# Performance work log

Hardware: AMD Instinct MI355X
Metric: run time of the kernel (lower is better)

The kernel has to match this reference:

```python
import jax, jax.numpy as jnp
import numpy as np

EPS = 1e-5
NEG_SLOPE = 0.01

def leaky_relu(x):
    return jnp.where(x > 0, x, NEG_SLOPE * x)

def graph_conv(x, src, dst, ew, W, n_nodes):
    # DGL GraphConv, norm='both', bias=False, with edge_weight.
    ones = jnp.ones(src.shape[0], dtype=x.dtype)
    out_deg = jax.ops.segment_sum(ones, src, num_segments=n_nodes)
    in_deg = jax.ops.segment_sum(ones, dst, num_segments=n_nodes)
    out_n = jnp.where(out_deg > 0, out_deg, 1.0) ** -0.5
    in_n = jnp.where(in_deg > 0, in_deg, 1.0) ** -0.5
    xs = x * out_n[:, None]
    msg = xs[src] * ew[:, None]              # [E, F] gather + elementwise
    agg = jax.ops.segment_sum(msg, dst, num_segments=n_nodes)  # scatter-add
    return (agg * in_n[:, None]) @ W

def graph_norm(x, gamma, beta, alpha):
    # GraphNorm called without graph arg -> normalize over all nodes per feature
    mean = jnp.mean(x, axis=0, keepdims=True)
    sub = x - alpha * mean
    var = jnp.mean(sub * sub, axis=0, keepdims=True)
    return gamma * sub * jax.lax.rsqrt(var + EPS) + beta

def inst_norm(x):
    # InstanceNorm1d(affine=False) on 2D [B,C]: normalize each row over features
    m = jnp.mean(x, axis=1, keepdims=True)
    v = jnp.mean((x - m) ** 2, axis=1, keepdims=True)
    return (x - m) * jax.lax.rsqrt(v + EPS)

def segment_mean(x, seg, num_segments):
    s = jax.ops.segment_sum(x, seg, num_segments=num_segments)
    c = jax.ops.segment_sum(jnp.ones(x.shape[0], x.dtype), seg, num_segments=num_segments)
    return s / jnp.maximum(c, 1.0)[:, None]

def setup_inputs() -> dict:
    N, E, B = 50000, 800000, 50
    IN, H, OUT = 64, 128, 16
    key = jax.random.key(0)
    ks = jax.random.split(key, 16)
    inp = {
        "node_feats": jax.random.normal(ks[0], (N, IN), jnp.float32),
        "src": jax.random.randint(ks[1], (E,), 0, N, jnp.int32),
        "dst": jax.random.randint(ks[2], (E,), 0, N, jnp.int32),
        "edge_weight": jax.random.uniform(ks[3], (E,), jnp.float32),
        "graph_id": jnp.sort(jax.random.randint(ks[4], (N,), 0, B, jnp.int32)),
        "W1": jax.random.normal(ks[5], (IN, H), jnp.float32) * (2.0 / IN) ** 0.5,
        "gn1_gamma": jnp.ones((H,), jnp.float32),
        "gn1_beta": jnp.zeros((H,), jnp.float32),
        "gn1_alpha": jnp.ones((H,), jnp.float32),
        "W2": jax.random.normal(ks[6], (H, H // 2), jnp.float32) * (2.0 / H) ** 0.5,
        "gn2_gamma": jnp.ones((H // 2,), jnp.float32),
        "gn2_beta": jnp.zeros((H // 2,), jnp.float32),
        "gn2_alpha": jnp.ones((H // 2,), jnp.float32),
        "L1": jax.random.normal(ks[7], (H // 2, H // 4), jnp.float32) * (1.0 / (H // 2)) ** 0.5,
        "L2": jax.random.normal(ks[8], (H // 4, H // 8), jnp.float32) * (1.0 / (H // 4)) ** 0.5,
        "L3": jax.random.normal(ks[9], (H // 8, H // 16), jnp.float32) * (1.0 / (H // 8)) ** 0.5,
        "Wc": jax.random.normal(ks[10], (H // 16, OUT), jnp.float32) * (1.0 / (H // 16)) ** 0.5,
    }
    return inp

def reference(node_feats, src, dst, edge_weight, graph_id,
              W1, gn1_gamma, gn1_beta, gn1_alpha,
              W2, gn2_gamma, gn2_beta, gn2_alpha,
              L1, L2, L3, Wc):
    N = node_feats.shape[0]
    B = 50
    h = graph_conv(node_feats, src, dst, edge_weight, W1, N)
    h = graph_norm(leaky_relu(h), gn1_gamma, gn1_beta, gn1_alpha)
    h = graph_conv(h, src, dst, edge_weight, W2, N)
    h = graph_norm(leaky_relu(h), gn2_gamma, gn2_beta, gn2_alpha)
    g = segment_mean(h, graph_id, B)          # mean_nodes readout -> [B, H/2]
    g = inst_norm(leaky_relu(g @ L1))          # dropout is identity in eval
    g = inst_norm(leaky_relu(g @ L2))
    g = inst_norm(leaky_relu(g @ L3))
    return g @ Wc
```

## Files before the change

### kernel.cpp

```cpp
#include <hip/hip_runtime.h>
#include <hip/hip_bf16.h>

#define NEG_SLOPE 0.01f
#define EPS 1e-5f

__device__ __forceinline__ float leaky(float x){ return x > 0.f ? x : NEG_SLOPE * x; }

__global__ void deg_kernel(const int* __restrict__ src, const int* __restrict__ dst,
                           int* __restrict__ iout, int* __restrict__ iin, int E){
  int e = blockIdx.x * blockDim.x + threadIdx.x;
  if (e < E){
    atomicAdd(&iout[src[e]], 1);
    atomicAdd(&iin[dst[e]], 1);
  }
}

__global__ void norm_kernel(const int* __restrict__ iout, const int* __restrict__ iin,
                            float* __restrict__ out_n, float* __restrict__ in_n, int N){
  int i = blockIdx.x * blockDim.x + threadIdx.x;
  if (i < N){
    int a = iout[i], b = iin[i];
    out_n[i] = rsqrtf((float)(a > 0 ? a : 1));
    in_n[i]  = rsqrtf((float)(b > 0 ? b : 1));
  }
}

__global__ __launch_bounds__(256) void scan_blocksum(const int* __restrict__ iin,
                                                     int* __restrict__ bsum, int N){
  __shared__ int sm[256];
  int t = threadIdx.x;
  int i = blockIdx.x * 256 + t;
  sm[t] = (i < N) ? iin[i] : 0;
  __syncthreads();
  for (int off = 128; off > 0; off >>= 1){
    if (t < off) sm[t] += sm[t + off];
    __syncthreads();
  }
  if (t == 0) bsum[blockIdx.x] = sm[0];
}

__global__ __launch_bounds__(1024) void scan_offsets(const int* __restrict__ bsum,
    int* __restrict__ boff, int nb, int* __restrict__ row_ptr, int N){
  __shared__ int sm[1024];
  int t = threadIdx.x;
  sm[t] = (t < nb) ? bsum[t] : 0;
  __syncthreads();
  for (int off = 1; off < 1024; off <<= 1){
    int v = (t >= off) ? sm[t - off] : 0;
    __syncthreads();
    sm[t] += v;
    __syncthreads();
  }
  if (t < nb) boff[t] = (t == 0) ? 0 : sm[t - 1];
  if (t == 1023) row_ptr[N] = sm[1023];
}

__global__ __launch_bounds__(256) void scan_write(const int* __restrict__ iin,
    const int* __restrict__ boff, int* __restrict__ row_ptr, int* __restrict__ cursor, int N){
  __shared__ int sm[256];
  int t = threadIdx.x;
  int i = blockIdx.x * 256 + t;
  int v = (i < N) ? iin[i] : 0;
  sm[t] = v;
  __syncthreads();
  for (int off = 1; off < 256; off <<= 1){
    int u = (t >= off) ? sm[t - off] : 0;
    __syncthreads();
    sm[t] += u;
    __syncthreads();
  }
  int excl = sm[t] - v + boff[blockIdx.x];
  if (i < N){ row_ptr[i] = excl; cursor[i] = excl; }
}

__global__ void fill_kernel(const int* __restrict__ src, const int* __restrict__ dst,
                            const float* __restrict__ ew, int* __restrict__ cursor,
                            int* __restrict__ esrc, float* __restrict__ eww, int E){
  int e = blockIdx.x * blockDim.x + threadIdx.x;
  if (e < E){
    int d = dst[e];
    int pos = atomicAdd(&cursor[d], 1);
    esrc[pos] = src[e];
    eww[pos] = ew[e];
  }
}

template<int MODE>
__global__ __launch_bounds__(256) void agg_csr(const float* __restrict__ xin,
    const int* __restrict__ row_ptr, const int* __restrict__ esrc,
    const float* __restrict__ eww, const float* __restrict__ out_n,
    const float* __restrict__ in_n, float* __restrict__ outp, int N){
  int node = (int)((blockIdx.x * (unsigned)blockDim.x + threadIdx.x) >> 6);
  int f = threadIdx.x & 63;
  if (node >= N) return;
  int e0 = row_ptr[node], e1 = row_ptr[node + 1];
  float acc = 0.f;
  #pragma unroll 2
  for (int e = e0; e < e1; ++e){
    int s = esrc[e];
    float w = eww[e];
    if (MODE == 1) w *= out_n[s];
    acc += xin[(size_t)s * 64 + f] * w;
  }
  acc *= in_n[node];
  if (MODE == 2) acc = leaky(acc);
  outp[(size_t)node * 64 + f] = acc;
}

__global__ __launch_bounds__(256) void gemm1_kernel(const float* __restrict__ agg,
    const float* __restrict__ W1, float* __restrict__ h1, int N){
  __shared__ float sW[64 * 128];
  __shared__ float sIn[64][64];
  int t = threadIdx.x;
  for (int i = t; i < 64 * 128 / 4; i += 256)
    ((float4*)sW)[i] = ((const float4*)W1)[i];
  int r0 = blockIdx.x * 64;
  for (int i = t; i < 64 * 16; i += 256){
    int r = i >> 4, q = i & 15;
    int row = r0 + r;
    float4 v = make_float4(0.f, 0.f, 0.f, 0.f);
    if (row < N) v = ((const float4*)(agg + (size_t)row * 64))[q];
    ((float4*)&sIn[r][0])[q] = v;
  }
  __syncthreads();
  int cp = t & 63;
  int rg = t >> 6;
  float2 acc[16];
  #pragma unroll
  for (int j = 0; j < 16; ++j) acc[j] = make_float2(0.f, 0.f);
  const float2* sW2 = (const float2*)sW;
  for (int k = 0; k < 64; k += 4){
    float2 w0 = sW2[(k + 0) * 64 + cp];
    float2 w1 = sW2[(k + 1) * 64 + cp];
    float2 w2 = sW2[(k + 2) * 64 + cp];
    float2 w3 = sW2[(k + 3) * 64 + cp];
    #pragma unroll
    for (int j = 0; j < 16; ++j){
      float4 a = *(const float4*)&sIn[rg * 16 + j][k];
      acc[j].x += a.x * w0.x + a.y * w1.x + a.z * w2.x + a.w * w3.x;
      acc[j].y += a.x * w0.y + a.y * w1.y + a.z * w2.y + a.w * w3.y;
    }
  }
  #pragma unroll
  for (int j = 0; j < 16; ++j){
    int row = r0 + rg * 16 + j;
    if (row < N){
      float2 o = make_float2(leaky(acc[j].x), leaky(acc[j].y));
      ((float2*)(h1 + (size_t)row * 128))[cp] = o;
    }
  }
}

template<int F>
__global__ void colstats_kernel(const float* __restrict__ h, int N,
                                float* __restrict__ sum, float* __restrict__ sumsq){
  int f = threadIdx.x;
  float s = 0.f, s2 = 0.f;
  for (int r = blockIdx.x; r < N; r += gridDim.x){
    float v = h[(size_t)r * F + f];
    s += v; s2 += v * v;
  }
  atomicAdd(&sum[f], s);
  atomicAdd(&sumsq[f], s2);
}

__global__ void finalize_norm(const float* __restrict__ sum, const float* __restrict__ sumsq,
                              const float* __restrict__ gamma, const float* __restrict__ beta,
                              const float* __restrict__ alpha,
                              float* __restrict__ a, float* __restrict__ b, int F, float invN){
  int f = threadIdx.x;
  if (f < F){
    float m = sum[f] * invN;
    float ex2 = sumsq[f] * invN;
    float al = alpha[f];
    float var = ex2 - m * m * al * (2.f - al);
    float av = gamma[f] * rsqrtf(var + EPS);
    a[f] = av;
    b[f] = beta[f] - av * al * m;
  }
}

__global__ __launch_bounds__(256) void gemm2_kernel(const float* __restrict__ h1,
    const float* __restrict__ out_n, const float* __restrict__ a1, const float* __restrict__ b1,
    const float* __restrict__ W2, float* __restrict__ z, int N){
  __shared__ float sW[128 * 64];
  __shared__ float sIn[64][128];
  int t = threadIdx.x;
  for (int i = t; i < 128 * 64 / 4; i += 256)
    ((float4*)sW)[i] = ((const float4*)W2)[i];
  int r0 = blockIdx.x * 64;
  for (int i = t; i < 64 * 32; i += 256){
    int r = i >> 5, q = i & 31;
    int row = r0 + r;
    float4 v = make_float4(0.f, 0.f, 0.f, 0.f);
    if (row < N){
      float4 h  = ((const float4*)(h1 + (size_t)row * 128))[q];
      float4 av = ((const float4*)a1)[q];
      float4 bv = ((const float4*)b1)[q];
      float  on = out_n[row];
      v.x = (av.x * h.x + bv.x) * on;
      v.y = (av.y * h.y + bv.y) * on;
      v.z = (av.z * h.z + bv.z) * on;
      v.w = (av.w * h.w + bv.w) * on;
    }
    ((float4*)&sIn[r][0])[q] = v;
  }
  __syncthreads();
  int cp = t & 31;
  int rg = t >> 5;
  float2 acc[8];
  #pragma unroll
  for (int j = 0; j < 8; ++j) acc[j] = make_float2(0.f, 0.f);
  const float2* sW2 = (const float2*)sW;
  for (int k = 0; k < 128; k += 4){
    float2 w0 = sW2[(k + 0) * 32 + cp];
    float2 w1 = sW2[(k + 1) * 32 + cp];
    float2 w2 = sW2[(k + 2) * 32 + cp];
    float2 w3 = sW2[(k + 3) * 32 + cp];
    #pragma unroll
    for (int j = 0; j < 8; ++j){
      float4 a = *(const float4*)&sIn[rg * 8 + j][k];
      acc[j].x += a.x * w0.x + a.y * w1.x + a.z * w2.x + a.w * w3.x;
      acc[j].y += a.x * w0.y + a.y * w1.y + a.z * w2.y + a.w * w3.y;
    }
  }
  #pragma unroll
  for (int j = 0; j < 8; ++j){
    int row = r0 + rg * 8 + j;
    if (row < N) ((float2*)(z + (size_t)row * 64))[cp] = acc[j];
  }
}

__global__ void post2_kernel(const float* __restrict__ hv, const int* __restrict__ gid,
                             int N, int chunk,
                             float* __restrict__ sum2, float* __restrict__ sumsq2,
                             float* __restrict__ segsum, float* __restrict__ cnt){
  int f = threadIdx.x;
  int r0 = blockIdx.x * chunk;
  int r1 = min(N, r0 + chunk);
  if (r0 >= r1) return;
  float s = 0.f, s2 = 0.f;
  int cur = gid[r0];
  float seg = 0.f;
  int run = 0;
  for (int r = r0; r < r1; ++r){
    int g = gid[r];
    if (g != cur){
      atomicAdd(&segsum[(size_t)cur * 64 + f], seg);
      if (f == 0) atomicAdd(&cnt[cur], (float)run);
      seg = 0.f; run = 0; cur = g;
    }
    float v = hv[(size_t)r * 64 + f];
    s += v; s2 += v * v;
    seg += v; ++run;
  }
  atomicAdd(&segsum[(size_t)cur * 64 + f], seg);
  if (f == 0) atomicAdd(&cnt[cur], (float)run);
  atomicAdd(&sum2[f], s);
  atomicAdd(&sumsq2[f], s2);
}

__global__ void head_kernel(const float* __restrict__ segsum, const float* __restrict__ cnt,
                            const float* __restrict__ a2, const float* __restrict__ b2,
                            const float* __restrict__ L1, const float* __restrict__ L2,
                            const float* __restrict__ L3, const float* __restrict__ Wc,
                            float* __restrict__ out){
  __shared__ float bufA[64];
  __shared__ float bufB[32];
  __shared__ float bufC[8];
  int b = blockIdx.x;
  int j = threadIdx.x;
  float c = cnt[b];
  float g0 = (c > 0.f) ? (a2[j] * (segsum[(size_t)b * 64 + j] / c) + b2[j]) : 0.f;
  bufA[j] = g0;
  __syncthreads();
  float y = 0.f;
  if (j < 32){
    float acc = 0.f;
    for (int f = 0; f < 64; ++f) acc += bufA[f] * L1[f * 32 + j];
    y = leaky(acc);
  }
  float m = y;
  for (int mask = 1; mask <= 16; mask <<= 1) m += __shfl_xor(m, mask);
  m *= (1.f / 32.f);
  float d = y - m;
  float v = d * d;
  for (int mask = 1; mask <= 16; mask <<= 1) v += __shfl_xor(v, mask);
  v *= (1.f / 32.f);
  float yn = d * rsqrtf(v + EPS);
  if (j < 32) bufB[j] = yn;
  __syncthreads();
  y = 0.f;
  if (j < 16){
    float acc = 0.f;
    for (int f = 0; f < 32; ++f) acc += bufB[f] * L2[f * 16 + j];
    y = leaky(acc);
  }
  m = y;
  for (int mask = 1; mask <= 8; mask <<= 1) m += __shfl_xor(m, mask);
  m *= (1.f / 16.f);
  d = y - m; v = d * d;
  for (int mask = 1; mask <= 8; mask <<= 1) v += __shfl_xor(v, mask);
  v *= (1.f / 16.f);
  yn = d * rsqrtf(v + EPS);
  if (j < 16) bufA[j] = yn;
  __syncthreads();
  y = 0.f;
  if (j < 8){
    float acc = 0.f;
    for (int f = 0; f < 16; ++f) acc += bufA[f] * L3[f * 8 + j];
    y = leaky(acc);
  }
  m = y;
  for (int mask = 1; mask <= 4; mask <<= 1) m += __shfl_xor(m, mask);
  m *= (1.f / 8.f);
  d = y - m; v = d * d;
  for (int mask = 1; mask <= 4; mask <<= 1) v += __shfl_xor(v, mask);
  v *= (1.f / 8.f);
  yn = d * rsqrtf(v + EPS);
  if (j < 8) bufC[j] = yn;
  __syncthreads();
  if (j < 16){
    float acc = 0.f;
    for (int f = 0; f < 8; ++f) acc += bufC[f] * Wc[f * 16 + j];
    out[(size_t)b * 16 + j] = acc;
  }
}

extern "C" void kernel_launch(void* const* d_in, const int* in_sizes, int n_in,
                              void* d_out, int out_size, void* d_ws, size_t ws_size,
                              hipStream_t stream){
  const float* x   = (const float*)d_in[0];
  const int*   src = (const int*)  d_in[1];
  const int*   dst = (const int*)  d_in[2];
  const float* ew  = (const float*)d_in[3];
  const int*   gid = (const int*)  d_in[4];
  const float* W1  = (const float*)d_in[5];
  const float* g1  = (const float*)d_in[6];
  const float* be1 = (const float*)d_in[7];
  const float* al1 = (const float*)d_in[8];
  const float* W2  = (const float*)d_in[9];
  const float* g2  = (const float*)d_in[10];
  const float* be2 = (const float*)d_in[11];
  const float* al2 = (const float*)d_in[12];
  const float* L1  = (const float*)d_in[13];
  const float* L2  = (const float*)d_in[14];
  const float* L3  = (const float*)d_in[15];
  const float* Wc  = (const float*)d_in[16];
  int N = in_sizes[0] / 64;
  int E = in_sizes[1];
  const int B = 50;
  int nb = (N + 255) / 256;

  char* wsb = (char*)d_ws;
  size_t off = 0;
  int* iout    = (int*)(wsb + off); off += sizeof(int) * (size_t)N;
  int* iin     = (int*)(wsb + off); off += sizeof(int) * (size_t)N;
  int* row_ptr = (int*)(wsb + off); off += sizeof(int) * ((size_t)N + 1);
  int* bsum    = (int*)(wsb + off); off += sizeof(int) * 1024;
  int* boff    = (int*)(wsb + off); off += sizeof(int) * 1024;
  int* esrc    = (int*)(wsb + off); off += sizeof(int) * (size_t)E;
  float* eww   = (float*)(wsb + off); off += sizeof(float) * (size_t)E;
  float* out_n = (float*)(wsb + off); off += sizeof(float) * (size_t)N;
  float* in_n  = (float*)(wsb + off); off += sizeof(float) * (size_t)N;
  float* P     = (float*)(wsb + off); off += sizeof(float) * (size_t)N * 64;
  float* H     = (float*)(wsb + off); off += sizeof(float) * (size_t)N * 128;
  float* sum1  = (float*)(wsb + off); off += sizeof(float) * 128;
  float* sumsq1= (float*)(wsb + off); off += sizeof(float) * 128;
  float* a1    = (float*)(wsb + off); off += sizeof(float) * 128;
  float* b1    = (float*)(wsb + off); off += sizeof(float) * 128;
  float* sum2  = (float*)(wsb + off); off += sizeof(float) * 64;
  float* sumsq2= (float*)(wsb + off); off += sizeof(float) * 64;
  float* a2    = (float*)(wsb + off); off += sizeof(float) * 64;
  float* b2    = (float*)(wsb + off); off += sizeof(float) * 64;
  float* segsum= (float*)(wsb + off); off += sizeof(float) * (size_t)B * 64;
  float* cnt   = (float*)(wsb + off); off += sizeof(float) * B;
  int* cursor  = iout;

  hipMemsetAsync(iout, 0, sizeof(int) * (size_t)2 * N, stream);
  hipMemsetAsync(sum1, 0, sizeof(float) * (4 * 128 + 4 * 64 + (size_t)B * 64 + B), stream);

  deg_kernel <<<(E + 255) / 256, 256, 0, stream>>>(src, dst, iout, iin, E);
  norm_kernel<<<(N + 255) / 256, 256, 0, stream>>>(iout, iin, out_n, in_n, N);
  scan_blocksum<<<nb, 256, 0, stream>>>(iin, bsum, N);
  scan_offsets <<<1, 1024, 0, stream>>>(bsum, boff, nb, row_ptr, N);
  scan_write   <<<nb, 256, 0, stream>>>(iin, boff, row_ptr, cursor, N);
  fill_kernel<<<(E + 255) / 256, 256, 0, stream>>>(src, dst, ew, cursor, esrc, eww, E);

  agg_csr<1><<<(N * 64 + 255) / 256, 256, 0, stream>>>(x, row_ptr, esrc, eww, out_n, in_n, P, N);
  gemm1_kernel<<<(N + 63) / 64, 256, 0, stream>>>(P, W1, H, N);
  colstats_kernel<128><<<256, 128, 0, stream>>>(H, N, sum1, sumsq1);
  finalize_norm<<<1, 128, 0, stream>>>(sum1, sumsq1, g1, be1, al1, a1, b1, 128, 1.f / (float)N);

  gemm2_kernel<<<(N + 63) / 64, 256, 0, stream>>>(H, out_n, a1, b1, W2, P, N);
  agg_csr<2><<<(N * 64 + 255) / 256, 256, 0, stream>>>(P, row_ptr, esrc, eww, nullptr, in_n, H, N);

  int chunk = (N + 1023) / 1024;
  post2_kernel<<<1024, 64, 0, stream>>>(H, gid, N, chunk, sum2, sumsq2, segsum, cnt);
  finalize_norm<<<1, 64, 0, stream>>>(sum2, sumsq2, g2, be2, al2, a2, b2, 64, 1.f / (float)N);

  head_kernel<<<B, 64, 0, stream>>>(segsum, cnt, a2, b2, L1, L2, L3, Wc, (float*)d_out);
}
```

Measured before the change: 492.7 us.

## Build CSR with per-chunk LDS histograms instead of global atomics

Replaces the global-atomic degree count and cursor-based CSR fill with a chunked scheme. Each of 64 edge chunks builds a packed 16-bit-per-node histogram in shared memory, and the chunks are reduced and prefix-scanned per node. A second pass fills the CSR using LDS atomics for local rank plus the per-chunk exclusive offsets. This removes contended global atomics but uses only 64-128 blocks with about 100KB of LDS each, which limits parallelism. The 16-bit counters overflow if a node has 65536 or more edges inside one chunk.

```diff
diff --git a/kernel.cpp b/kernel.cpp
--- a/kernel.cpp
+++ b/kernel.cpp
@@ -3,25 +3,64 @@
 
 #define NEG_SLOPE 0.01f
 #define EPS 1e-5f
+#define NCHUNK 64
+#define MAXW 25088
 
 __device__ __forceinline__ float leaky(float x){ return x > 0.f ? x : NEG_SLOPE * x; }
 
-__global__ void deg_kernel(const int* __restrict__ src, const int* __restrict__ dst,
-                           int* __restrict__ iout, int* __restrict__ iin, int E){
-  int e = blockIdx.x * blockDim.x + threadIdx.x;
-  if (e < E){
-    atomicAdd(&iout[src[e]], 1);
-    atomicAdd(&iin[dst[e]], 1);
-  }
-}
-
-__global__ void norm_kernel(const int* __restrict__ iout, const int* __restrict__ iin,
-                            float* __restrict__ out_n, float* __restrict__ in_n, int N){
-  int i = blockIdx.x * blockDim.x + threadIdx.x;
-  if (i < N){
-    int a = iout[i], b = iin[i];
-    out_n[i] = rsqrtf((float)(a > 0 ? a : 1));
-    in_n[i]  = rsqrtf((float)(b > 0 ? b : 1));
+__global__ __launch_bounds__(256) void hist_kernel(const int* __restrict__ src,
+    const int* __restrict__ dst, int E, int ECH, int W,
+    unsigned* __restrict__ partial_out, unsigned* __restrict__ partial_in){
+  __shared__ unsigned sm[MAXW];
+  int t = threadIdx.x;
+  int c = blockIdx.x >> 1;
+  int which = blockIdx.x & 1;
+  for (int i = t; i < W; i += 256) sm[i] = 0u;
+  __syncthreads();
+  const int* ids = which ? dst : src;
+  int e0 = c * ECH, e1 = min(E, e0 + ECH);
+  for (int e = e0 + t; e < e1; e += 256){
+    int v = ids[e];
+    atomicAdd(&sm[v >> 1], 1u << ((v & 1) * 16));
+  }
+  __syncthreads();
+  unsigned* outp = (which ? partial_in : partial_out) + (size_t)c * W;
+  for (int i = t; i < W; i += 256) outp[i] = sm[i];
+}
+
+__global__ void reduce_kernel(const unsigned* __restrict__ partial_out,
+    const unsigned* __restrict__ partial_in, int W, int N,
+    float* __restrict__ out_n, float* __restrict__ in_n, int* __restrict__ iin){
+  int w = blockIdx.x * blockDim.x + threadIdx.x;
+  if (w >= W) return;
+  unsigned so = 0, si = 0;
+  for (int c = 0; c < NCHUNK; ++c){
+    so += partial_out[(size_t)c * W + w];
+    si += partial_in[(size_t)c * W + w];
+  }
+  int n0 = 2 * w, n1 = 2 * w + 1;
+  int o0 = so & 0xffff, o1 = so >> 16;
+  int i0 = si & 0xffff, i1 = si >> 16;
+  if (n0 < N){
+    out_n[n0] = rsqrtf((float)(o0 > 0 ? o0 : 1));
+    in_n[n0]  = rsqrtf((float)(i0 > 0 ? i0 : 1));
+    iin[n0] = i0;
+  }
+  if (n1 < N){
+    out_n[n1] = rsqrtf((float)(o1 > 0 ? o1 : 1));
+    in_n[n1]  = rsqrtf((float)(i1 > 0 ? i1 : 1));
+    iin[n1] = i1;
+  }
+}
+
+__global__ void pexcl_kernel(unsigned* __restrict__ partial_in, int W){
+  int w = blockIdx.x * blockDim.x + threadIdx.x;
+  if (w >= W) return;
+  unsigned run = 0;
+  for (int c = 0; c < NCHUNK; ++c){
+    unsigned v = partial_in[(size_t)c * W + w];
+    partial_in[(size_t)c * W + w] = run;
+    run += v;
   }
 }
 
@@ -56,7 +95,7 @@
 }
 
 __global__ __launch_bounds__(256) void scan_write(const int* __restrict__ iin,
-    const int* __restrict__ boff, int* __restrict__ row_ptr, int* __restrict__ cursor, int N){
+    const int* __restrict__ boff, int* __restrict__ row_ptr, int N){
   __shared__ int sm[256];
   int t = threadIdx.x;
   int i = blockIdx.x * 256 + t;
@@ -69,17 +108,27 @@
     sm[t] += u;
     __syncthreads();
   }
-  int excl = sm[t] - v + boff[blockIdx.x];
-  if (i < N){ row_ptr[i] = excl; cursor[i] = excl; }
-}
-
-__global__ void fill_kernel(const int* __restrict__ src, const int* __restrict__ dst,
-                            const float* __restrict__ ew, int* __restrict__ cursor,
-                            int* __restrict__ esrc, float* __restrict__ eww, int E){
-  int e = blockIdx.x * blockDim.x + threadIdx.x;
-  if (e < E){
+  if (i < N) row_ptr[i] = sm[t] - v + boff[blockIdx.x];
+}
+
+__global__ __launch_bounds__(256) void fill2_kernel(const int* __restrict__ src,
+    const int* __restrict__ dst, const float* __restrict__ ew,
+    const int* __restrict__ row_ptr, const unsigned* __restrict__ pexcl,
+    int E, int ECH, int W, int* __restrict__ esrc, float* __restrict__ eww){
+  __shared__ unsigned sm[MAXW];
+  int t = threadIdx.x;
+  int c = blockIdx.x;
+  for (int i = t; i < W; i += 256) sm[i] = 0u;
+  __syncthreads();
+  const unsigned* pe = pexcl + (size_t)c * W;
+  int e0 = c * ECH, e1 = min(E, e0 + ECH);
+  for (int e = e0 + t; e < e1; e += 256){
     int d = dst[e];
-    int pos = atomicAdd(&cursor[d], 1);
+    int sh = (d & 1) * 16;
+    unsigned old = atomicAdd(&sm[d >> 1], 1u << sh);
+    int rank = (int)((old >> sh) & 0xffffu);
+    int base = (int)((pe[d >> 1] >> sh) & 0xffffu);
+    int pos = row_ptr[d] + base + rank;
     esrc[pos] = src[e];
     eww[pos] = ew[e];
   }
@@ -351,10 +400,11 @@
   int E = in_sizes[1];
   const int B = 50;
   int nb = (N + 255) / 256;
+  int W = (N + 1) / 2;
+  int ECH = (E + NCHUNK - 1) / NCHUNK;
 
   char* wsb = (char*)d_ws;
   size_t off = 0;
-  int* iout    = (int*)(wsb + off); off += sizeof(int) * (size_t)N;
   int* iin     = (int*)(wsb + off); off += sizeof(int) * (size_t)N;
   int* row_ptr = (int*)(wsb + off); off += sizeof(int) * ((size_t)N + 1);
   int* bsum    = (int*)(wsb + off); off += sizeof(int) * 1024;
@@ -375,17 +425,18 @@
   float* b2    = (float*)(wsb + off); off += sizeof(float) * 64;
   float* segsum= (float*)(wsb + off); off += sizeof(float) * (size_t)B * 64;
   float* cnt   = (float*)(wsb + off); off += sizeof(float) * B;
-  int* cursor  = iout;
-
-  hipMemsetAsync(iout, 0, sizeof(int) * (size_t)2 * N, stream);
+  unsigned* partial_out = (unsigned*)H;
+  unsigned* partial_in  = partial_out + (size_t)NCHUNK * W;
+
   hipMemsetAsync(sum1, 0, sizeof(float) * (4 * 128 + 4 * 64 + (size_t)B * 64 + B), stream);
 
-  deg_kernel <<<(E + 255) / 256, 256, 0, stream>>>(src, dst, iout, iin, E);
-  norm_kernel<<<(N + 255) / 256, 256, 0, stream>>>(iout, iin, out_n, in_n, N);
+  hist_kernel <<<NCHUNK * 2, 256, 0, stream>>>(src, dst, E, ECH, W, partial_out, partial_in);
+  reduce_kernel<<<(W + 255) / 256, 256, 0, stream>>>(partial_out, partial_in, W, N, out_n, in_n, iin);
   scan_blocksum<<<nb, 256, 0, stream>>>(iin, bsum, N);
   scan_offsets <<<1, 1024, 0, stream>>>(bsum, boff, nb, row_ptr, N);
-  scan_write   <<<nb, 256, 0, stream>>>(iin, boff, row_ptr, cursor, N);
-  fill_kernel<<<(E + 255) / 256, 256, 0, stream>>>(src, dst, ew, cursor, esrc, eww, E);
+  scan_write   <<<nb, 256, 0, stream>>>(iin, boff, row_ptr, N);
+  pexcl_kernel <<<(W + 255) / 256, 256, 0, stream>>>(partial_in, W);
+  fill2_kernel <<<NCHUNK, 256, 0, stream>>>(src, dst, ew, row_ptr, partial_in, E, ECH, W, esrc, eww);
 
   agg_csr<1><<<(N * 64 + 255) / 256, 256, 0, stream>>>(x, row_ptr, esrc, eww, out_n, in_n, P, N);
   gemm1_kernel<<<(N + 63) / 64, 256, 0, stream>>>(P, W1, H, N);
```

New measurement: 463.9 us. 1.06x faster.
